# Performance work log

Hardware: AMD Instinct MI355X
Metric: run time of the kernel (lower is better)

The kernel has to match this reference:

```python
import jax, jax.numpy as jnp
import numpy as np

N_NODES = 100000
N_EDGES = 1600000
NFEAT, NHID, NCLASS, NL = 128, 64, 40, 6


def setup_inputs() -> dict:
    key = jax.random.key(0)
    ks = jax.random.split(key, 12)
    x = jax.random.normal(ks[0], (N_NODES, NFEAT), dtype=jnp.float32)
    edge_row = jax.random.randint(ks[1], (N_EDGES,), 0, N_NODES)
    edge_col = jax.random.randint(ks[2], (N_EDGES,), 0, N_NODES)
    # positive values mimicking a degree-normalized adjacency
    edge_val = jax.random.uniform(ks[3], (N_EDGES,), dtype=jnp.float32) / 16.0
    s1 = 1.0 / np.sqrt(NFEAT)
    sh = 1.0 / np.sqrt(NHID)
    W1 = jax.random.uniform(ks[4], (NFEAT, NHID), minval=-s1, maxval=s1, dtype=jnp.float32)
    b1 = jax.random.uniform(ks[5], (NHID,), minval=-s1, maxval=s1, dtype=jnp.float32)
    Wm = jax.random.uniform(ks[6], (NL, NHID, NHID), minval=-sh, maxval=sh, dtype=jnp.float32)
    bm = jax.random.uniform(ks[7], (NL, NHID), minval=-sh, maxval=sh, dtype=jnp.float32)
    W2 = jax.random.uniform(ks[8], (NHID, NCLASS), minval=-sh, maxval=sh, dtype=jnp.float32)
    b2 = jax.random.uniform(ks[9], (NCLASS,), minval=-sh, maxval=sh, dtype=jnp.float32)
    return {"x": x, "edge_row": edge_row, "edge_col": edge_col, "edge_val": edge_val,
            "W1": W1, "b1": b1, "Wm": Wm, "bm": bm, "W2": W2, "b2": b2}


def _gconv(h, row, col, val, W, b):
    # GraphConvolution: support = h @ W ; out = spmm(adj, support) + b
    support = h @ W                       # [N, out]
    msgs = val[:, None] * support[col]    # [E, out] gather
    agg = jax.ops.segment_sum(msgs, row, num_segments=h.shape[0])  # scatter-add
    return agg + b


def reference(x, edge_row, edge_col, edge_val, W1, b1, Wm, bm, W2, b2):
    # gc1: relu (dropout is identity in eval mode)
    h1 = jax.nn.relu(_gconv(x, edge_row, edge_col, edge_val, W1, b1))
    # first middle layer (module index 2): relu, no residual
    h2 = jax.nn.relu(_gconv(h1, edge_row, edge_col, edge_val, Wm[0], bm[0]))
    prev2, prev = h1, h2
    # remaining middle layers: relu + residual to two layers back
    for k in range(1, NL):
        h = jax.nn.relu(_gconv(prev, edge_row, edge_col, edge_val, Wm[k], bm[k])) + prev2
        prev2, prev = prev, h
    out = _gconv(prev, edge_row, edge_col, edge_val, W2, b2)  # gc2, no relu
    return jax.nn.log_softmax(out, axis=1)
```

## Files before the change

### kernel.cpp

```cpp
#include <hip/hip_runtime.h>
#include <hip/hip_bf16.h>
#include <math.h>

#define N_NODES 100000
#define N_EDGES 1600000
#define NFEAT 128
#define NHID  64
#define NCLASS 40
#define NL 6

#define NBUK 256
#define RPB  391
#define EPP  (N_EDGES / NBUK)
#define EP_PAD 256
#define NTILES (N_NODES / 16)

typedef __attribute__((ext_vector_type(8))) short short8;
typedef __attribute__((ext_vector_type(4))) float floatx4;

__device__ __forceinline__ float bfbits(unsigned short u) {
  return __uint_as_float((unsigned int)u << 16);
}
__device__ __forceinline__ short f2bs(float f) {
  __hip_bfloat16 h = __float2bfloat16(f);
  return *reinterpret_cast<short*>(&h);
}

__global__ __launch_bounds__(256) void p0_hist_k(const int* __restrict__ row,
                                                 int* __restrict__ h2d) {
  __shared__ int h[NBUK];
  const int i = blockIdx.x, t = threadIdx.x;
  h[t] = 0;
  __syncthreads();
  const int e0 = i * EPP, e1 = e0 + EPP;
  for (int e = e0 + t; e < e1; e += 256) atomicAdd(&h[row[e] / RPB], 1);
  __syncthreads();
  h2d[i * NBUK + t] = h[t];
}

__global__ __launch_bounds__(256) void k1_scanb_k(int* __restrict__ h2d,
                                                  int* __restrict__ btot) {
  __shared__ int sd[256];
  const int b = blockIdx.x, t = threadIdx.x;
  int v = h2d[t * NBUK + b];
  sd[t] = v;
  __syncthreads();
  for (int off = 1; off < 256; off <<= 1) {
    int a = (t >= off) ? sd[t - off] : 0;
    __syncthreads();
    sd[t] += a;
    __syncthreads();
  }
  h2d[t * NBUK + b] = sd[t] - v;
  if (t == 255) btot[b] = sd[255];
}

__global__ __launch_bounds__(256) void k2_scanbase_k(const int* __restrict__ btot,
                                                     int* __restrict__ bbase,
                                                     int2* __restrict__ ep) {
  __shared__ int sd[256];
  const int t = threadIdx.x;
  int v = btot[t];
  sd[t] = v;
  __syncthreads();
  for (int off = 1; off < 256; off <<= 1) {
    int a = (t >= off) ? sd[t - off] : 0;
    __syncthreads();
    sd[t] += a;
    __syncthreads();
  }
  bbase[t] = sd[t] - v;
  if (t == 255) bbase[256] = sd[255];
  if (t < EP_PAD) ep[N_EDGES + t] = make_int2(0, 0);
}

__global__ __launch_bounds__(256) void p2_part_k(
    const int* __restrict__ row, const int* __restrict__ col,
    const float* __restrict__ val, const int* __restrict__ h2d,
    const int* __restrict__ bbase, int2* __restrict__ pcv,
    unsigned short* __restrict__ plr) {
  __shared__ int cur[NBUK];
  const int i = blockIdx.x, t = threadIdx.x;
  cur[t] = bbase[t] + h2d[i * NBUK + t];
  __syncthreads();
  const int e0 = i * EPP, e1 = e0 + EPP;
  for (int e = e0 + t; e < e1; e += 256) {
    int r = row[e];
    int b = r / RPB;
    int p = atomicAdd(&cur[b], 1);
    pcv[p] = make_int2(col[e], __float_as_int(val[e]));
    plr[p] = (unsigned short)(r - b * RPB);
  }
}

__global__ __launch_bounds__(256) void p3_fine_k(const int2* __restrict__ pcv,
                                                 const unsigned short* __restrict__ plr,
                                                 const int* __restrict__ bbase,
                                                 int* __restrict__ rp,
                                                 int2* __restrict__ ep) {
  __shared__ int cnt[RPB];
  __shared__ int cur[RPB];
  const int b = blockIdx.x, t = threadIdx.x;
  const int ebeg = bbase[b], eend = bbase[b + 1];
  const int r0 = b * RPB;
  const int nloc = min(RPB, N_NODES - r0);

  for (int i = t; i < RPB; i += 256) cnt[i] = 0;
  __syncthreads();
  for (int j = ebeg + t; j < eend; j += 256) atomicAdd(&cnt[plr[j]], 1);
  __syncthreads();

  if (t < 64) {
    const int base_ = t * 7;
    int v[7], s = 0;
#pragma unroll
    for (int k = 0; k < 7; ++k) {
      int idx = base_ + k;
      v[k] = (idx < RPB) ? cnt[idx] : 0;
      s += v[k];
    }
    int incl = s;
#pragma unroll
    for (int off = 1; off < 64; off <<= 1) {
      int y = __shfl_up(incl, off);
      if (t >= off) incl += y;
    }
    int run = incl - s;
#pragma unroll
    for (int k = 0; k < 7; ++k) {
      int idx = base_ + k;
      if (idx < RPB) cnt[idx] = run;
      run += v[k];
    }
  }
  __syncthreads();

  for (int i = t; i < nloc; i += 256) {
    rp[r0 + i] = ebeg + cnt[i];
    cur[i] = cnt[i];
  }
  if (b == 0 && t == 0) rp[N_NODES] = N_EDGES;
  __syncthreads();

  for (int j = ebeg + t; j < eend; j += 256) {
    int lr = plr[j];
    int p = atomicAdd(&cur[lr], 1);
    ep[ebeg + p] = pcv[j];
  }
}

__global__ __launch_bounds__(256) void gemm_l1(const float* __restrict__ X,
                                               const float* __restrict__ W,
                                               unsigned short* __restrict__ S) {
  const int lane = threadIdx.x & 63;
  const int quad = lane >> 4;
  const int m = lane & 15;

  short8 bf[4][4];
#pragma unroll
  for (int t = 0; t < 4; ++t)
#pragma unroll
    for (int h = 0; h < 4; ++h)
#pragma unroll
      for (int j = 0; j < 8; ++j)
        bf[t][h][j] = f2bs(W[(h * 32 + quad * 8 + j) * 64 + t * 16 + m]);

  const int wid = blockIdx.x * 4 + (threadIdx.x >> 6);
  for (int tile = wid; tile < NTILES; tile += gridDim.x * 4) {
    const int r0 = tile * 16;
    const float* xr = X + (size_t)(r0 + m) * 128;
    short8 af[4];
#pragma unroll
    for (int h = 0; h < 4; ++h) {
      const float* p = xr + h * 32 + quad * 8;
      float4 a = *(const float4*)p;
      float4 b = *(const float4*)(p + 4);
      af[h][0] = f2bs(a.x); af[h][1] = f2bs(a.y);
      af[h][2] = f2bs(a.z); af[h][3] = f2bs(a.w);
      af[h][4] = f2bs(b.x); af[h][5] = f2bs(b.y);
      af[h][6] = f2bs(b.z); af[h][7] = f2bs(b.w);
    }
#pragma unroll
    for (int t = 0; t < 4; ++t) {
      floatx4 acc = {0.0f, 0.0f, 0.0f, 0.0f};
#pragma unroll
      for (int h = 0; h < 4; ++h)
        acc = __builtin_amdgcn_mfma_f32_16x16x32_bf16(af[h], bf[t][h], acc, 0, 0, 0);
#pragma unroll
      for (int r = 0; r < 4; ++r)
        S[(size_t)(r0 + quad * 4 + r) * 64 + t * 16 + m] = (unsigned short)f2bs(acc[r]);
    }
  }
}

template <int COLS>
__global__ __launch_bounds__(256) void gemm_bf(const unsigned short* __restrict__ Hb,
                                               const float* __restrict__ W,
                                               unsigned short* __restrict__ S) {
  const int lane = threadIdx.x & 63;
  const int quad = lane >> 4;
  const int m = lane & 15;

  short8 bf[4][2];
#pragma unroll
  for (int t = 0; t < 4; ++t) {
    const int cc = t * 16 + m;
#pragma unroll
    for (int h = 0; h < 2; ++h)
#pragma unroll
      for (int j = 0; j < 8; ++j)
        bf[t][h][j] = (COLS == 64 || cc < COLS)
                          ? f2bs(W[(h * 32 + quad * 8 + j) * COLS + cc])
                          : (short)0;
  }

  const int wid = blockIdx.x * 4 + (threadIdx.x >> 6);
  for (int tile = wid; tile < NTILES; tile += gridDim.x * 4) {
    const int r0 = tile * 16;
    const unsigned short* hr = Hb + (size_t)(r0 + m) * 64 + quad * 8;
    short8 af0 = *(const short8*)hr;
    short8 af1 = *(const short8*)(hr + 32);
#pragma unroll
    for (int t = 0; t < 4; ++t) {
      floatx4 acc = {0.0f, 0.0f, 0.0f, 0.0f};
      acc = __builtin_amdgcn_mfma_f32_16x16x32_bf16(af0, bf[t][0], acc, 0, 0, 0);
      acc = __builtin_amdgcn_mfma_f32_16x16x32_bf16(af1, bf[t][1], acc, 0, 0, 0);
#pragma unroll
      for (int r = 0; r < 4; ++r)
        S[(size_t)(r0 + quad * 4 + r) * 64 + t * 16 + m] = (unsigned short)f2bs(acc[r]);
    }
  }
}

template <bool RES, bool STOREF>
__global__ __launch_bounds__(256) void spmm16_k(
    const unsigned short* __restrict__ S, const int2* __restrict__ ep,
    const int* __restrict__ rp, const float* __restrict__ bias,
    const float* __restrict__ res, float* __restrict__ Hout,
    unsigned short* __restrict__ Hbout) {
  const int lane = threadIdx.x & 63;
  const int g = lane >> 4;
  const int i16 = lane & 15;
  const int gl = g & 1;
  const int pair = blockIdx.x * 4 + (threadIdx.x >> 6);
  const int nodeA = pair * 2;
  const int sA = rp[nodeA], sB = rp[nodeA + 1], eB = rp[nodeA + 2];
  const bool isB = (g >= 2);
  const int myNode = nodeA + (isB ? 1 : 0);
  const int myEnd = isB ? eB : sB;
  const int iters = (max(sB - sA, eB - sB) + 7) >> 3;

  const int foff = i16 * 4;

  float a0 = 0.0f, a1 = 0.0f, a2 = 0.0f, a3 = 0.0f;
  int e = (isB ? sB : sA) + gl * 2;
  for (int it = 0; it < iters; ++it, e += 8) {
    const int o0 = e, o1 = e + 1, o2 = e + 4, o3 = e + 5;
    int2 q0 = ep[o0];
    int2 q1 = ep[o1];
    int2 q2 = ep[o2];
    int2 q3 = ep[o3];
    float v0 = (o0 < myEnd) ? __int_as_float(q0.y) : 0.0f;
    float v1 = (o1 < myEnd) ? __int_as_float(q1.y) : 0.0f;
    float v2 = (o2 < myEnd) ? __int_as_float(q2.y) : 0.0f;
    float v3 = (o3 < myEnd) ? __int_as_float(q3.y) : 0.0f;
    ushort4 s0 = *(const ushort4*)(S + ((q0.x << 6) + foff));
    ushort4 s1 = *(const ushort4*)(S + ((q1.x << 6) + foff));
    ushort4 s2 = *(const ushort4*)(S + ((q2.x << 6) + foff));
    ushort4 s3 = *(const ushort4*)(S + ((q3.x << 6) + foff));
    a0 = fmaf(v0, bfbits(s0.x), a0); a1 = fmaf(v0, bfbits(s0.y), a1);
    a2 = fmaf(v0, bfbits(s0.z), a2); a3 = fmaf(v0, bfbits(s0.w), a3);
    a0 = fmaf(v1, bfbits(s1.x), a0); a1 = fmaf(v1, bfbits(s1.y), a1);
    a2 = fmaf(v1, bfbits(s1.z), a2); a3 = fmaf(v1, bfbits(s1.w), a3);
    a0 = fmaf(v2, bfbits(s2.x), a0); a1 = fmaf(v2, bfbits(s2.y), a1);
    a2 = fmaf(v2, bfbits(s2.z), a2); a3 = fmaf(v2, bfbits(s2.w), a3);
    a0 = fmaf(v3, bfbits(s3.x), a0); a1 = fmaf(v3, bfbits(s3.y), a1);
    a2 = fmaf(v3, bfbits(s3.z), a2); a3 = fmaf(v3, bfbits(s3.w), a3);
  }

  a0 += __shfl_xor(a0, 16);
  a1 += __shfl_xor(a1, 16);
  a2 += __shfl_xor(a2, 16);
  a3 += __shfl_xor(a3, 16);

  if ((g & 1) == 0) {
    float4 b4 = ((const float4*)bias)[i16];
    float h0 = fmaxf(a0 + b4.x, 0.0f);
    float h1 = fmaxf(a1 + b4.y, 0.0f);
    float h2 = fmaxf(a2 + b4.z, 0.0f);
    float h3 = fmaxf(a3 + b4.w, 0.0f);
    if (RES) {
      float4 r4 = ((const float4*)res)[myNode * 16 + i16];
      h0 += r4.x; h1 += r4.y; h2 += r4.z; h3 += r4.w;
    }
    if (STOREF)
      ((float4*)Hout)[myNode * 16 + i16] = make_float4(h0, h1, h2, h3);
    ushort4 hb;
    hb.x = (unsigned short)f2bs(h0);
    hb.y = (unsigned short)f2bs(h1);
    hb.z = (unsigned short)f2bs(h2);
    hb.w = (unsigned short)f2bs(h3);
    ((ushort4*)Hbout)[myNode * 16 + i16] = hb;
  }
}

__global__ __launch_bounds__(256) void spmm_final_k(
    const unsigned short* __restrict__ S, const int2* __restrict__ ep,
    const int* __restrict__ rp, const float* __restrict__ b2,
    float* __restrict__ out) {
  const int lane = threadIdx.x & 63;
  const int g = lane >> 4;
  const int i16 = lane & 15;
  const int gl = g & 1;
  const int pair = blockIdx.x * 4 + (threadIdx.x >> 6);
  const int nodeA = pair * 2;
  const int sA = rp[nodeA], sB = rp[nodeA + 1], eB = rp[nodeA + 2];
  const bool isB = (g >= 2);
  const int myNode = nodeA + (isB ? 1 : 0);
  const int myEnd = isB ? eB : sB;
  const int iters = (max(sB - sA, eB - sB) + 7) >> 3;

  const int foff = i16 * 4;

  float a0 = 0.0f, a1 = 0.0f, a2 = 0.0f, a3 = 0.0f;
  int e = (isB ? sB : sA) + gl * 2;
  for (int it = 0; it < iters; ++it, e += 8) {
    const int o0 = e, o1 = e + 1, o2 = e + 4, o3 = e + 5;
    int2 q0 = ep[o0];
    int2 q1 = ep[o1];
    int2 q2 = ep[o2];
    int2 q3 = ep[o3];
    float v0 = (o0 < myEnd) ? __int_as_float(q0.y) : 0.0f;
    float v1 = (o1 < myEnd) ? __int_as_float(q1.y) : 0.0f;
    float v2 = (o2 < myEnd) ? __int_as_float(q2.y) : 0.0f;
    float v3 = (o3 < myEnd) ? __int_as_float(q3.y) : 0.0f;
    ushort4 s0 = *(const ushort4*)(S + ((q0.x << 6) + foff));
    ushort4 s1 = *(const ushort4*)(S + ((q1.x << 6) + foff));
    ushort4 s2 = *(const ushort4*)(S + ((q2.x << 6) + foff));
    ushort4 s3 = *(const ushort4*)(S + ((q3.x << 6) + foff));
    a0 = fmaf(v0, bfbits(s0.x), a0); a1 = fmaf(v0, bfbits(s0.y), a1);
    a2 = fmaf(v0, bfbits(s0.z), a2); a3 = fmaf(v0, bfbits(s0.w), a3);
    a0 = fmaf(v1, bfbits(s1.x), a0); a1 = fmaf(v1, bfbits(s1.y), a1);
    a2 = fmaf(v1, bfbits(s1.z), a2); a3 = fmaf(v1, bfbits(s1.w), a3);
    a0 = fmaf(v2, bfbits(s2.x), a0); a1 = fmaf(v2, bfbits(s2.y), a1);
    a2 = fmaf(v2, bfbits(s2.z), a2); a3 = fmaf(v2, bfbits(s2.w), a3);
    a0 = fmaf(v3, bfbits(s3.x), a0); a1 = fmaf(v3, bfbits(s3.y), a1);
    a2 = fmaf(v3, bfbits(s3.z), a2); a3 = fmaf(v3, bfbits(s3.w), a3);
  }
  a0 += __shfl_xor(a0, 16);
  a1 += __shfl_xor(a1, 16);
  a2 += __shfl_xor(a2, 16);
  a3 += __shfl_xor(a3, 16);

  const bool valid = (i16 < 10);
  float l0 = -INFINITY, l1 = -INFINITY, l2 = -INFINITY, l3 = -INFINITY;
  if (valid) {
    float4 b4 = ((const float4*)b2)[i16];
    l0 = a0 + b4.x; l1 = a1 + b4.y; l2 = a2 + b4.z; l3 = a3 + b4.w;
  }
  float mx = fmaxf(fmaxf(l0, l1), fmaxf(l2, l3));
#pragma unroll
  for (int off = 1; off < 16; off <<= 1) mx = fmaxf(mx, __shfl_xor(mx, off));
  float sum = valid ? (expf(l0 - mx) + expf(l1 - mx) + expf(l2 - mx) + expf(l3 - mx)) : 0.0f;
#pragma unroll
  for (int off = 1; off < 16; off <<= 1) sum += __shfl_xor(sum, off);
  if (((g & 1) == 0) && valid) {
    float lg = logf(sum);
    ((float4*)out)[myNode * 10 + i16] =
        make_float4(l0 - mx - lg, l1 - mx - lg, l2 - mx - lg, l3 - mx - lg);
  }
}

extern "C" void kernel_launch(void* const* d_in, const int* in_sizes, int n_in,
                              void* d_out, int out_size, void* d_ws, size_t ws_size,
                              hipStream_t stream) {
  const float* x    = (const float*)d_in[0];
  const int*   erow = (const int*)d_in[1];
  const int*   ecol = (const int*)d_in[2];
  const float* eval = (const float*)d_in[3];
  const float* W1   = (const float*)d_in[4];
  const float* b1   = (const float*)d_in[5];
  const float* Wm   = (const float*)d_in[6];
  const float* bm   = (const float*)d_in[7];
  const float* W2   = (const float*)d_in[8];
  const float* b2   = (const float*)d_in[9];
  float* out = (float*)d_out;

  char* ws = (char*)d_ws;
  size_t off = 0;
  auto alloc = [&](size_t bytes) {
    void* p = ws + off;
    off = (off + bytes + 255) & ~(size_t)255;
    return p;
  };
  int*  rp    = (int*)alloc((N_NODES + 1) * sizeof(int));
  int*  h2d   = (int*)alloc((size_t)NBUK * NBUK * sizeof(int));
  int*  btot  = (int*)alloc(NBUK * sizeof(int));
  int*  bbase = (int*)alloc((NBUK + 1) * sizeof(int));
  int2* ep    = (int2*)alloc((size_t)(N_EDGES + EP_PAD) * sizeof(int2));
  char* U     = (char*)alloc((size_t)N_EDGES * sizeof(int2) +
                             (((size_t)N_EDGES * sizeof(unsigned short) + 255) & ~(size_t)255));
  int2* pcv = (int2*)U;
  unsigned short* plr = (unsigned short*)(U + (size_t)N_EDGES * sizeof(int2));
  unsigned short* S = (unsigned short*)U;
  float* F0 = (float*)alloc((size_t)N_NODES * 64 * sizeof(float));
  float* F1 = (float*)alloc((size_t)N_NODES * 64 * sizeof(float));
  unsigned short* Hb = (unsigned short*)alloc((size_t)N_NODES * 64 * sizeof(unsigned short));

  const int SPMM_GRID = N_NODES / 8;
  const int GEMM_GRID = 512;

  p0_hist_k<<<NBUK, 256, 0, stream>>>(erow, h2d);
  k1_scanb_k<<<NBUK, 256, 0, stream>>>(h2d, btot);
  k2_scanbase_k<<<1, 256, 0, stream>>>(btot, bbase, ep);
  p2_part_k<<<NBUK, 256, 0, stream>>>(erow, ecol, eval, h2d, bbase, pcv, plr);
  p3_fine_k<<<NBUK, 256, 0, stream>>>(pcv, plr, bbase, rp, ep);

  gemm_l1<<<GEMM_GRID, 256, 0, stream>>>(x, W1, S);
  spmm16_k<false, true><<<SPMM_GRID, 256, 0, stream>>>(S, ep, rp, b1, nullptr, F0, Hb);

  gemm_bf<64><<<GEMM_GRID, 256, 0, stream>>>(Hb, Wm, S);
  spmm16_k<false, true><<<SPMM_GRID, 256, 0, stream>>>(S, ep, rp, bm, nullptr, F1, Hb);

  gemm_bf<64><<<GEMM_GRID, 256, 0, stream>>>(Hb, Wm + 1 * 4096, S);
  spmm16_k<true, true><<<SPMM_GRID, 256, 0, stream>>>(S, ep, rp, bm + 1 * 64, F0, F0, Hb);

  gemm_bf<64><<<GEMM_GRID, 256, 0, stream>>>(Hb, Wm + 2 * 4096, S);
  spmm16_k<true, true><<<SPMM_GRID, 256, 0, stream>>>(S, ep, rp, bm + 2 * 64, F1, F1, Hb);

  gemm_bf<64><<<GEMM_GRID, 256, 0, stream>>>(Hb, Wm + 3 * 4096, S);
  spmm16_k<true, true><<<SPMM_GRID, 256, 0, stream>>>(S, ep, rp, bm + 3 * 64, F0, F0, Hb);

  gemm_bf<64><<<GEMM_GRID, 256, 0, stream>>>(Hb, Wm + 4 * 4096, S);
  spmm16_k<true, false><<<SPMM_GRID, 256, 0, stream>>>(S, ep, rp, bm + 4 * 64, F1, nullptr, Hb);

  gemm_bf<64><<<GEMM_GRID, 256, 0, stream>>>(Hb, Wm + 5 * 4096, S);
  spmm16_k<true, false><<<SPMM_GRID, 256, 0, stream>>>(S, ep, rp, bm + 5 * 64, F0, nullptr, Hb);

  gemm_bf<40><<<GEMM_GRID, 256, 0, stream>>>(Hb, W2, S);
  spmm_final_k<<<SPMM_GRID, 256, 0, stream>>>(S, ep, rp, b2, out);
}
```

Measured before the change: 565.5 us.

## Widen SpMM gathers to 16-byte rows, prefetch edges, keep residuals in bf16

The SpMM kernels now have each 8-lane group gather a full 128-byte bf16 row with 16-byte loads. Edge descriptors are prefetched one iteration ahead, and the cross-lane reduction uses two xor shuffles. The fp32 residual buffers are dropped: residuals are read back from ping-pong bf16 buffers that are updated in place, which cuts global traffic but adds bf16 rounding error to the residual chain. The CSR preprocessing kernels also move from 256 to 1024 threads per block.

```diff
diff --git a/kernel.cpp b/kernel.cpp
--- a/kernel.cpp
+++ b/kernel.cpp
@@ -16,6 +16,7 @@
 #define NTILES (N_NODES / 16)
 
 typedef __attribute__((ext_vector_type(8))) short short8;
+typedef __attribute__((ext_vector_type(8))) unsigned short ushort8v;
 typedef __attribute__((ext_vector_type(4))) float floatx4;
 
 __device__ __forceinline__ float bfbits(unsigned short u) {
@@ -26,16 +27,16 @@
   return *reinterpret_cast<short*>(&h);
 }
 
-__global__ __launch_bounds__(256) void p0_hist_k(const int* __restrict__ row,
-                                                 int* __restrict__ h2d) {
+__global__ __launch_bounds__(1024) void p0_hist_k(const int* __restrict__ row,
+                                                  int* __restrict__ h2d) {
   __shared__ int h[NBUK];
   const int i = blockIdx.x, t = threadIdx.x;
-  h[t] = 0;
+  if (t < NBUK) h[t] = 0;
   __syncthreads();
   const int e0 = i * EPP, e1 = e0 + EPP;
-  for (int e = e0 + t; e < e1; e += 256) atomicAdd(&h[row[e] / RPB], 1);
-  __syncthreads();
-  h2d[i * NBUK + t] = h[t];
+  for (int e = e0 + t; e < e1; e += 1024) atomicAdd(&h[row[e] / RPB], 1);
+  __syncthreads();
+  if (t < NBUK) h2d[i * NBUK + t] = h[t];
 }
 
 __global__ __launch_bounds__(256) void k1_scanb_k(int* __restrict__ h2d,
@@ -74,17 +75,17 @@
   if (t < EP_PAD) ep[N_EDGES + t] = make_int2(0, 0);
 }
 
-__global__ __launch_bounds__(256) void p2_part_k(
+__global__ __launch_bounds__(1024) void p2_part_k(
     const int* __restrict__ row, const int* __restrict__ col,
     const float* __restrict__ val, const int* __restrict__ h2d,
     const int* __restrict__ bbase, int2* __restrict__ pcv,
     unsigned short* __restrict__ plr) {
   __shared__ int cur[NBUK];
   const int i = blockIdx.x, t = threadIdx.x;
-  cur[t] = bbase[t] + h2d[i * NBUK + t];
+  if (t < NBUK) cur[t] = bbase[t] + h2d[i * NBUK + t];
   __syncthreads();
   const int e0 = i * EPP, e1 = e0 + EPP;
-  for (int e = e0 + t; e < e1; e += 256) {
+  for (int e = e0 + t; e < e1; e += 1024) {
     int r = row[e];
     int b = r / RPB;
     int p = atomicAdd(&cur[b], 1);
@@ -93,11 +94,11 @@
   }
 }
 
-__global__ __launch_bounds__(256) void p3_fine_k(const int2* __restrict__ pcv,
-                                                 const unsigned short* __restrict__ plr,
-                                                 const int* __restrict__ bbase,
-                                                 int* __restrict__ rp,
-                                                 int2* __restrict__ ep) {
+__global__ __launch_bounds__(1024) void p3_fine_k(const int2* __restrict__ pcv,
+                                                  const unsigned short* __restrict__ plr,
+                                                  const int* __restrict__ bbase,
+                                                  int* __restrict__ rp,
+                                                  int2* __restrict__ ep) {
   __shared__ int cnt[RPB];
   __shared__ int cur[RPB];
   const int b = blockIdx.x, t = threadIdx.x;
@@ -105,9 +106,9 @@
   const int r0 = b * RPB;
   const int nloc = min(RPB, N_NODES - r0);
 
-  for (int i = t; i < RPB; i += 256) cnt[i] = 0;
-  __syncthreads();
-  for (int j = ebeg + t; j < eend; j += 256) atomicAdd(&cnt[plr[j]], 1);
+  for (int i = t; i < RPB; i += 1024) cnt[i] = 0;
+  __syncthreads();
+  for (int j = ebeg + t; j < eend; j += 1024) atomicAdd(&cnt[plr[j]], 1);
   __syncthreads();
 
   if (t < 64) {
@@ -135,14 +136,14 @@
   }
   __syncthreads();
 
-  for (int i = t; i < nloc; i += 256) {
+  for (int i = t; i < nloc; i += 1024) {
     rp[r0 + i] = ebeg + cnt[i];
     cur[i] = cnt[i];
   }
   if (b == 0 && t == 0) rp[N_NODES] = N_EDGES;
   __syncthreads();
 
-  for (int j = ebeg + t; j < eend; j += 256) {
+  for (int j = ebeg + t; j < eend; j += 1024) {
     int lr = plr[j];
     int p = atomicAdd(&cur[lr], 1);
     ep[ebeg + p] = pcv[j];
@@ -232,75 +233,63 @@
   }
 }
 
-template <bool RES, bool STOREF>
-__global__ __launch_bounds__(256) void spmm16_k(
+template <bool RES>
+__global__ __launch_bounds__(256) void spmm8_k(
     const unsigned short* __restrict__ S, const int2* __restrict__ ep,
     const int* __restrict__ rp, const float* __restrict__ bias,
-    const float* __restrict__ res, float* __restrict__ Hout,
     unsigned short* __restrict__ Hbout) {
   const int lane = threadIdx.x & 63;
-  const int g = lane >> 4;
-  const int i16 = lane & 15;
-  const int gl = g & 1;
+  const int og = lane >> 3;
+  const int i8 = lane & 7;
+  const int sg = og & 3;
+  const bool isB = og >= 4;
   const int pair = blockIdx.x * 4 + (threadIdx.x >> 6);
   const int nodeA = pair * 2;
   const int sA = rp[nodeA], sB = rp[nodeA + 1], eB = rp[nodeA + 2];
-  const bool isB = (g >= 2);
   const int myNode = nodeA + (isB ? 1 : 0);
+  const int myBeg = isB ? sB : sA;
   const int myEnd = isB ? eB : sB;
   const int iters = (max(sB - sA, eB - sB) + 7) >> 3;
 
-  const int foff = i16 * 4;
-
-  float a0 = 0.0f, a1 = 0.0f, a2 = 0.0f, a3 = 0.0f;
-  int e = (isB ? sB : sA) + gl * 2;
-  for (int it = 0; it < iters; ++it, e += 8) {
-    const int o0 = e, o1 = e + 1, o2 = e + 4, o3 = e + 5;
-    int2 q0 = ep[o0];
-    int2 q1 = ep[o1];
-    int2 q2 = ep[o2];
-    int2 q3 = ep[o3];
-    float v0 = (o0 < myEnd) ? __int_as_float(q0.y) : 0.0f;
-    float v1 = (o1 < myEnd) ? __int_as_float(q1.y) : 0.0f;
-    float v2 = (o2 < myEnd) ? __int_as_float(q2.y) : 0.0f;
-    float v3 = (o3 < myEnd) ? __int_as_float(q3.y) : 0.0f;
-    ushort4 s0 = *(const ushort4*)(S + ((q0.x << 6) + foff));
-    ushort4 s1 = *(const ushort4*)(S + ((q1.x << 6) + foff));
-    ushort4 s2 = *(const ushort4*)(S + ((q2.x << 6) + foff));
-    ushort4 s3 = *(const ushort4*)(S + ((q3.x << 6) + foff));
-    a0 = fmaf(v0, bfbits(s0.x), a0); a1 = fmaf(v0, bfbits(s0.y), a1);
-    a2 = fmaf(v0, bfbits(s0.z), a2); a3 = fmaf(v0, bfbits(s0.w), a3);
-    a0 = fmaf(v1, bfbits(s1.x), a0); a1 = fmaf(v1, bfbits(s1.y), a1);
-    a2 = fmaf(v1, bfbits(s1.z), a2); a3 = fmaf(v1, bfbits(s1.w), a3);
-    a0 = fmaf(v2, bfbits(s2.x), a0); a1 = fmaf(v2, bfbits(s2.y), a1);
-    a2 = fmaf(v2, bfbits(s2.z), a2); a3 = fmaf(v2, bfbits(s2.w), a3);
-    a0 = fmaf(v3, bfbits(s3.x), a0); a1 = fmaf(v3, bfbits(s3.y), a1);
-    a2 = fmaf(v3, bfbits(s3.z), a2); a3 = fmaf(v3, bfbits(s3.w), a3);
-  }
-
-  a0 += __shfl_xor(a0, 16);
-  a1 += __shfl_xor(a1, 16);
-  a2 += __shfl_xor(a2, 16);
-  a3 += __shfl_xor(a3, 16);
-
-  if ((g & 1) == 0) {
-    float4 b4 = ((const float4*)bias)[i16];
-    float h0 = fmaxf(a0 + b4.x, 0.0f);
-    float h1 = fmaxf(a1 + b4.y, 0.0f);
-    float h2 = fmaxf(a2 + b4.z, 0.0f);
-    float h3 = fmaxf(a3 + b4.w, 0.0f);
+  float a[8] = {0, 0, 0, 0, 0, 0, 0, 0};
+  int e = myBeg + sg;
+  int2 q0 = ep[e], q1 = ep[e + 4];
+  for (int it = 0; it < iters; ++it) {
+    int2 n0 = ep[e + 8], n1 = ep[e + 12];
+    float v0 = (e < myEnd) ? __int_as_float(q0.y) : 0.0f;
+    float v1 = (e + 4 < myEnd) ? __int_as_float(q1.y) : 0.0f;
+    ushort8v s0 = *(const ushort8v*)(S + ((size_t)q0.x * 64 + i8 * 8));
+    ushort8v s1 = *(const ushort8v*)(S + ((size_t)q1.x * 64 + i8 * 8));
+#pragma unroll
+    for (int j = 0; j < 8; ++j) a[j] = fmaf(v0, bfbits(s0[j]), a[j]);
+#pragma unroll
+    for (int j = 0; j < 8; ++j) a[j] = fmaf(v1, bfbits(s1[j]), a[j]);
+    q0 = n0; q1 = n1; e += 8;
+  }
+
+#pragma unroll
+  for (int j = 0; j < 8; ++j) {
+    a[j] += __shfl_xor(a[j], 8);
+    a[j] += __shfl_xor(a[j], 16);
+  }
+
+  if (sg == 0) {
+    float4 b0 = ((const float4*)bias)[i8 * 2];
+    float4 b1 = ((const float4*)bias)[i8 * 2 + 1];
+    float h[8];
+    h[0] = fmaxf(a[0] + b0.x, 0.0f); h[1] = fmaxf(a[1] + b0.y, 0.0f);
+    h[2] = fmaxf(a[2] + b0.z, 0.0f); h[3] = fmaxf(a[3] + b0.w, 0.0f);
+    h[4] = fmaxf(a[4] + b1.x, 0.0f); h[5] = fmaxf(a[5] + b1.y, 0.0f);
+    h[6] = fmaxf(a[6] + b1.z, 0.0f); h[7] = fmaxf(a[7] + b1.w, 0.0f);
     if (RES) {
-      float4 r4 = ((const float4*)res)[myNode * 16 + i16];
-      h0 += r4.x; h1 += r4.y; h2 += r4.z; h3 += r4.w;
-    }
-    if (STOREF)
-      ((float4*)Hout)[myNode * 16 + i16] = make_float4(h0, h1, h2, h3);
-    ushort4 hb;
-    hb.x = (unsigned short)f2bs(h0);
-    hb.y = (unsigned short)f2bs(h1);
-    hb.z = (unsigned short)f2bs(h2);
-    hb.w = (unsigned short)f2bs(h3);
-    ((ushort4*)Hbout)[myNode * 16 + i16] = hb;
+      ushort8v r = ((const ushort8v*)Hbout)[(size_t)myNode * 8 + i8];
+#pragma unroll
+      for (int j = 0; j < 8; ++j) h[j] += bfbits(r[j]);
+    }
+    ushort8v hb;
+#pragma unroll
+    for (int j = 0; j < 8; ++j) hb[j] = (unsigned short)f2bs(h[j]);
+    ((ushort8v*)Hbout)[(size_t)myNode * 8 + i8] = hb;
   }
 }
 
@@ -309,65 +298,67 @@
     const int* __restrict__ rp, const float* __restrict__ b2,
     float* __restrict__ out) {
   const int lane = threadIdx.x & 63;
-  const int g = lane >> 4;
-  const int i16 = lane & 15;
-  const int gl = g & 1;
+  const int og = lane >> 3;
+  const int i8 = lane & 7;
+  const int sg = og & 3;
+  const bool isB = og >= 4;
   const int pair = blockIdx.x * 4 + (threadIdx.x >> 6);
   const int nodeA = pair * 2;
   const int sA = rp[nodeA], sB = rp[nodeA + 1], eB = rp[nodeA + 2];
-  const bool isB = (g >= 2);
   const int myNode = nodeA + (isB ? 1 : 0);
+  const int myBeg = isB ? sB : sA;
   const int myEnd = isB ? eB : sB;
   const int iters = (max(sB - sA, eB - sB) + 7) >> 3;
 
-  const int foff = i16 * 4;
-
-  float a0 = 0.0f, a1 = 0.0f, a2 = 0.0f, a3 = 0.0f;
-  int e = (isB ? sB : sA) + gl * 2;
-  for (int it = 0; it < iters; ++it, e += 8) {
-    const int o0 = e, o1 = e + 1, o2 = e + 4, o3 = e + 5;
-    int2 q0 = ep[o0];
-    int2 q1 = ep[o1];
-    int2 q2 = ep[o2];
-    int2 q3 = ep[o3];
-    float v0 = (o0 < myEnd) ? __int_as_float(q0.y) : 0.0f;
-    float v1 = (o1 < myEnd) ? __int_as_float(q1.y) : 0.0f;
-    float v2 = (o2 < myEnd) ? __int_as_float(q2.y) : 0.0f;
-    float v3 = (o3 < myEnd) ? __int_as_float(q3.y) : 0.0f;
-    ushort4 s0 = *(const ushort4*)(S + ((q0.x << 6) + foff));
-    ushort4 s1 = *(const ushort4*)(S + ((q1.x << 6) + foff));
-    ushort4 s2 = *(const ushort4*)(S + ((q2.x << 6) + foff));
-    ushort4 s3 = *(const ushort4*)(S + ((q3.x << 6) + foff));
-    a0 = fmaf(v0, bfbits(s0.x), a0); a1 = fmaf(v0, bfbits(s0.y), a1);
-    a2 = fmaf(v0, bfbits(s0.z), a2); a3 = fmaf(v0, bfbits(s0.w), a3);
-    a0 = fmaf(v1, bfbits(s1.x), a0); a1 = fmaf(v1, bfbits(s1.y), a1);
-    a2 = fmaf(v1, bfbits(s1.z), a2); a3 = fmaf(v1, bfbits(s1.w), a3);
-    a0 = fmaf(v2, bfbits(s2.x), a0); a1 = fmaf(v2, bfbits(s2.y), a1);
-    a2 = fmaf(v2, bfbits(s2.z), a2); a3 = fmaf(v2, bfbits(s2.w), a3);
-    a0 = fmaf(v3, bfbits(s3.x), a0); a1 = fmaf(v3, bfbits(s3.y), a1);
-    a2 = fmaf(v3, bfbits(s3.z), a2); a3 = fmaf(v3, bfbits(s3.w), a3);
-  }
-  a0 += __shfl_xor(a0, 16);
-  a1 += __shfl_xor(a1, 16);
-  a2 += __shfl_xor(a2, 16);
-  a3 += __shfl_xor(a3, 16);
-
-  const bool valid = (i16 < 10);
-  float l0 = -INFINITY, l1 = -INFINITY, l2 = -INFINITY, l3 = -INFINITY;
+  float a[8] = {0, 0, 0, 0, 0, 0, 0, 0};
+  int e = myBeg + sg;
+  int2 q0 = ep[e], q1 = ep[e + 4];
+  for (int it = 0; it < iters; ++it) {
+    int2 n0 = ep[e + 8], n1 = ep[e + 12];
+    float v0 = (e < myEnd) ? __int_as_float(q0.y) : 0.0f;
+    float v1 = (e + 4 < myEnd) ? __int_as_float(q1.y) : 0.0f;
+    ushort8v s0 = *(const ushort8v*)(S + ((size_t)q0.x * 64 + i8 * 8));
+    ushort8v s1 = *(const ushort8v*)(S + ((size_t)q1.x * 64 + i8 * 8));
+#pragma unroll
+    for (int j = 0; j < 8; ++j) a[j] = fmaf(v0, bfbits(s0[j]), a[j]);
+#pragma unroll
+    for (int j = 0; j < 8; ++j) a[j] = fmaf(v1, bfbits(s1[j]), a[j]);
+    q0 = n0; q1 = n1; e += 8;
+  }
+
+#pragma unroll
+  for (int j = 0; j < 8; ++j) {
+    a[j] += __shfl_xor(a[j], 8);
+    a[j] += __shfl_xor(a[j], 16);
+  }
+
+  const bool valid = (i8 < 5);
+  float l[8];
+  float mx = -INFINITY;
   if (valid) {
-    float4 b4 = ((const float4*)b2)[i16];
-    l0 = a0 + b4.x; l1 = a1 + b4.y; l2 = a2 + b4.z; l3 = a3 + b4.w;
-  }
-  float mx = fmaxf(fmaxf(l0, l1), fmaxf(l2, l3));
-#pragma unroll
-  for (int off = 1; off < 16; off <<= 1) mx = fmaxf(mx, __shfl_xor(mx, off));
-  float sum = valid ? (expf(l0 - mx) + expf(l1 - mx) + expf(l2 - mx) + expf(l3 - mx)) : 0.0f;
-#pragma unroll
-  for (int off = 1; off < 16; off <<= 1) sum += __shfl_xor(sum, off);
-  if (((g & 1) == 0) && valid) {
-    float lg = logf(sum);
-    ((float4*)out)[myNode * 10 + i16] =
-        make_float4(l0 - mx - lg, l1 - mx - lg, l2 - mx - lg, l3 - mx - lg);
+    float4 c0 = ((const float4*)b2)[i8 * 2];
+    float4 c1 = ((const float4*)b2)[i8 * 2 + 1];
+    l[0] = a[0] + c0.x; l[1] = a[1] + c0.y; l[2] = a[2] + c0.z; l[3] = a[3] + c0.w;
+    l[4] = a[4] + c1.x; l[5] = a[5] + c1.y; l[6] = a[6] + c1.z; l[7] = a[7] + c1.w;
+#pragma unroll
+    for (int j = 0; j < 8; ++j) mx = fmaxf(mx, l[j]);
+  }
+#pragma unroll
+  for (int off = 1; off < 8; off <<= 1) mx = fmaxf(mx, __shfl_xor(mx, off));
+  float sum = 0.0f;
+  if (valid) {
+#pragma unroll
+    for (int j = 0; j < 8; ++j) sum += expf(l[j] - mx);
+  }
+#pragma unroll
+  for (int off = 1; off < 8; off <<= 1) sum += __shfl_xor(sum, off);
+
+  if (sg == 0 && valid) {
+    float lg = mx + logf(sum);
+    ((float4*)out)[(size_t)myNode * 10 + i8 * 2] =
+        make_float4(l[0] - lg, l[1] - lg, l[2] - lg, l[3] - lg);
+    ((float4*)out)[(size_t)myNode * 10 + i8 * 2 + 1] =
+        make_float4(l[4] - lg, l[5] - lg, l[6] - lg, l[7] - lg);
   }
 }
 
@@ -403,40 +394,39 @@
   int2* pcv = (int2*)U;
   unsigned short* plr = (unsigned short*)(U + (size_t)N_EDGES * sizeof(int2));
   unsigned short* S = (unsigned short*)U;
-  float* F0 = (float*)alloc((size_t)N_NODES * 64 * sizeof(float));
-  float* F1 = (float*)alloc((size_t)N_NODES * 64 * sizeof(float));
-  unsigned short* Hb = (unsigned short*)alloc((size_t)N_NODES * 64 * sizeof(unsigned short));
+  unsigned short* B0 = (unsigned short*)alloc((size_t)N_NODES * 64 * sizeof(unsigned short));
+  unsigned short* B1 = (unsigned short*)alloc((size_t)N_NODES * 64 * sizeof(unsigned short));
 
   const int SPMM_GRID = N_NODES / 8;
   const int GEMM_GRID = 512;
 
-  p0_hist_k<<<NBUK, 256, 0, stream>>>(erow, h2d);
+  p0_hist_k<<<NBUK, 1024, 0, stream>>>(erow, h2d);
   k1_scanb_k<<<NBUK, 256, 0, stream>>>(h2d, btot);
   k2_scanbase_k<<<1, 256, 0, stream>>>(btot, bbase, ep);
-  p2_part_k<<<NBUK, 256, 0, stream>>>(erow, ecol, eval, h2d, bbase, pcv, plr);
-  p3_fine_k<<<NBUK, 256, 0, stream>>>(pcv, plr, bbase, rp, ep);
+  p2_part_k<<<NBUK, 1024, 0, stream>>>(erow, ecol, eval, h2d, bbase, pcv, plr);
+  p3_fine_k<<<NBUK, 1024, 0, stream>>>(pcv, plr, bbase, rp, ep);
 
   gemm_l1<<<GEMM_GRID, 256, 0, stream>>>(x, W1, S);
-  spmm16_k<false, true><<<SPMM_GRID, 256, 0, stream>>>(S, ep, rp, b1, nullptr, F0, Hb);
-
-  gemm_bf<64><<<GEMM_GRID, 256, 0, stream>>>(Hb, Wm, S);
-  spmm16_k<false, true><<<SPMM_GRID, 256, 0, stream>>>(S, ep, rp, bm, nullptr, F1, Hb);
-
-  gemm_bf<64><<<GEMM_GRID, 256, 0, stream>>>(Hb, Wm + 1 * 4096, S);
-  spmm16_k<true, true><<<SPMM_GRID, 256, 0, stream>>>(S, ep, rp, bm + 1 * 64, F0, F0, Hb);
-
-  gemm_bf<64><<<GEMM_GRID, 256, 0, stream>>>(Hb, Wm + 2 * 4096, S);
-  spmm16_k<true, true><<<SPMM_GRID, 256, 0, stream>>>(S, ep, rp, bm + 2 * 64, F1, F1, Hb);
-
-  gemm_bf<64><<<GEMM_GRID, 256, 0, stream>>>(Hb, Wm + 3 * 4096, S);
-  spmm16_k<true, true><<<SPMM_GRID, 256, 0, stream>>>(S, ep, rp, bm + 3 * 64, F0, F0, Hb);
-
-  gemm_bf<64><<<GEMM_GRID, 256, 0, stream>>>(Hb, Wm + 4 * 4096, S);
-  spmm16_k<true, false><<<SPMM_GRID, 256, 0, stream>>>(S, ep, rp, bm + 4 * 64, F1, nullptr, Hb);
-
-  gemm_bf<64><<<GEMM_GRID, 256, 0, stream>>>(Hb, Wm + 5 * 4096, S);
-  spmm16_k<true, false><<<SPMM_GRID, 256, 0, stream>>>(S, ep, rp, bm + 5 * 64, F0, nullptr, Hb);
-
-  gemm_bf<40><<<GEMM_GRID, 256, 0, stream>>>(Hb, W2, S);
+  spmm8_k<false><<<SPMM_GRID, 256, 0, stream>>>(S, ep, rp, b1, B0);
+
+  gemm_bf<64><<<GEMM_GRID, 256, 0, stream>>>(B0, Wm, S);
+  spmm8_k<false><<<SPMM_GRID, 256, 0, stream>>>(S, ep, rp, bm, B1);
+
+  gemm_bf<64><<<GEMM_GRID, 256, 0, stream>>>(B1, Wm + 1 * 4096, S);
+  spmm8_k<true><<<SPMM_GRID, 256, 0, stream>>>(S, ep, rp, bm + 1 * 64, B0);
+
+  gemm_bf<64><<<GEMM_GRID, 256, 0, stream>>>(B0, Wm + 2 * 4096, S);
+  spmm8_k<true><<<SPMM_GRID, 256, 0, stream>>>(S, ep, rp, bm + 2 * 64, B1);
+
+  gemm_bf<64><<<GEMM_GRID, 256, 0, stream>>>(B1, Wm + 3 * 4096, S);
+  spmm8_k<true><<<SPMM_GRID, 256, 0, stream>>>(S, ep, rp, bm + 3 * 64, B0);
+
+  gemm_bf<64><<<GEMM_GRID, 256, 0, stream>>>(B0, Wm + 4 * 4096, S);
+  spmm8_k<true><<<SPMM_GRID, 256, 0, stream>>>(S, ep, rp, bm + 4 * 64, B1);
+
+  gemm_bf<64><<<GEMM_GRID, 256, 0, stream>>>(B1, Wm + 5 * 4096, S);
+  spmm8_k<true><<<SPMM_GRID, 256, 0, stream>>>(S, ep, rp, bm + 5 * 64, B0);
+
+  gemm_bf<40><<<GEMM_GRID, 256, 0, stream>>>(B0, W2, S);
   spmm_final_k<<<SPMM_GRID, 256, 0, stream>>>(S, ep, rp, b2, out);
 }
```

Result: faster. 511.6 us (-9.5%).
